# Optimization experiments

Measured on AMD Instinct MI355X. Metric: run time of the kernel, lower is better.

## Reference

```python
import jax, jax.numpy as jnp
import numpy as np

NUM_BITS = 1024
DIM = 128
SIGMA = 0.1
MU = 0.0


def setup_inputs() -> dict:
    key = jax.random.key(0)
    k1, k2, k3 = jax.random.split(key, 3)
    emb1 = jax.random.normal(k1, (4096, DIM), dtype=jnp.float32)
    emb2 = jax.random.normal(k2, (8192, DIM), dtype=jnp.float32)
    r = jax.random.normal(k3, (NUM_BITS, DIM), dtype=jnp.float32) * SIGMA + MU
    pi = jnp.array([np.pi], dtype=jnp.float32)
    return {"emb1": emb1, "emb2": emb2, "r": r, "pi": pi}


def reference(emb1, emb2, r, pi):
    d = r.shape[0]  # num_bits
    # LSH: random projection then binarize (sign bits as 0/1 floats)
    u = (emb1 @ r.T > 0).astype(jnp.float32)  # [N1, d]
    v = (emb2 @ r.T > 0).astype(jnp.float32)  # [N2, d]
    # cdist(p=0) on binary codes == Hamming distance.
    # For binary u,v: sum(u != v) = sum(u) + sum(v) - 2 * u @ v.T
    su = jnp.sum(u, axis=-1, keepdims=True)        # [N1, 1]
    sv = jnp.sum(v, axis=-1)                       # [N2]
    hamming = su + sv[None, :] - 2.0 * (u @ v.T)   # [N1, N2]
    return jnp.cos((pi[0] / d) * hamming)
```

## Files before the change

### kernel.cpp

```cpp
#include <hip/hip_runtime.h>
#include <hip/hip_bf16.h>
#include <stdint.h>


#define NBITS   1024
#define NROWS1  4096
#define NROWS2  8192

__global__ __launch_bounds__(256, 3) void lsh_project_pack(
    const float4* __restrict__ emb1,
    const float4* __restrict__ emb2,
    const float4* __restrict__ r4,
    unsigned long long* __restrict__ packed)
{
  __shared__ float4 e_lds[32 * 32];
  __shared__ float4 r_lds[256 * 8];

  const int t = threadIdx.x;
  const int w = t >> 6;
  const int l = t & 63;
  const int rowBlk  = blockIdx.x;
  const int bitTile = blockIdx.y;

  const int rowStart = rowBlk * 32;
  const bool side1   = rowStart < NROWS1;
  const float4* __restrict__ eb4 = side1 ? emb1 : emb2;
  const int rowOff = side1 ? rowStart : rowStart - NROWS1;

#pragma unroll
  for (int i = 0; i < 4; ++i) {
    const int idx = t + i * 256;
    e_lds[idx] = eb4[rowOff * 32 + idx];
  }

  float acc[8][4];
#pragma unroll
  for (int r = 0; r < 8; ++r)
#pragma unroll
    for (int p = 0; p < 4; ++p) acc[r][p] = 0.0f;

  const int key = l & 7;

  for (int ch = 0; ch < 4; ++ch) {
    __syncthreads();
#pragma unroll
    for (int i = 0; i < 8; ++i) {
      const int idx = t + i * 256;
      const int bit = idx >> 3;
      const int s   = idx & 7;
      r_lds[bit * 8 + (s ^ (bit & 7))] =
          r4[(size_t)(bitTile * 256 + bit) * 32 + ch * 8 + s];
    }
    __syncthreads();

#pragma unroll
    for (int ks = 0; ks < 8; ++ks) {
      float4 rv[4];
#pragma unroll
      for (int p = 0; p < 4; ++p)
        rv[p] = r_lds[(p * 64 + l) * 8 + (ks ^ key)];
      float4 ev[8];
#pragma unroll
      for (int r = 0; r < 8; ++r)
        ev[r] = e_lds[(w * 8 + r) * 32 + ch * 8 + ks];
#pragma unroll
      for (int r = 0; r < 8; ++r)
#pragma unroll
        for (int p = 0; p < 4; ++p) {
          acc[r][p] = fmaf(ev[r].x, rv[p].x, acc[r][p]);
          acc[r][p] = fmaf(ev[r].y, rv[p].y, acc[r][p]);
          acc[r][p] = fmaf(ev[r].z, rv[p].z, acc[r][p]);
          acc[r][p] = fmaf(ev[r].w, rv[p].w, acc[r][p]);
        }
    }
  }

  unsigned long long myword = 0;
#pragma unroll
  for (int r = 0; r < 8; ++r)
#pragma unroll
    for (int p = 0; p < 4; ++p) {
      const unsigned long long m = __ballot(acc[r][p] > 0.0f);
      if (l == r * 4 + p) myword = m;
    }
  if (l < 32) {
    const int row = rowStart + w * 8 + (l >> 2);
    packed[(size_t)row * 16 + bitTile * 4 + (l & 3)] = myword;
  }
}

__global__ __launch_bounds__(256, 3) void lsh_hamming_cos(
    const uint4* __restrict__ up,
    const uint4* __restrict__ vp,
    const float* __restrict__ pi_in,
    float* __restrict__ out)
{
  __shared__ uint4 u_lds[64 * 8];
  __shared__ uint4 v_lds[256 * 8];

  const int t  = threadIdx.x;
  const int w  = t >> 6;
  const int l  = t & 63;
  const int n0 = blockIdx.x * 256;
  const int m0 = blockIdx.y * 64;

#pragma unroll
  for (int i = 0; i < 2; ++i)
    u_lds[t + i * 256] = up[(size_t)m0 * 8 + t + i * 256];

#pragma unroll
  for (int i = 0; i < 8; ++i) {
    const int idx = t + i * 256;
    const int col = idx >> 3;
    const int w4  = idx & 7;
    v_lds[col * 8 + (w4 ^ ((col >> 2) & 7))] = vp[(size_t)n0 * 8 + idx];
  }
  __syncthreads();

  int h[8][8];
#pragma unroll
  for (int r = 0; r < 8; ++r)
#pragma unroll
    for (int j = 0; j < 8; ++j) h[r][j] = 0;

  const int key  = l & 7;
  const int row0 = w * 16 + (l >> 5) * 8;
  const int c0   = (l & 31) * 4;

#pragma unroll
  for (int kk = 0; kk < 8; ++kk) {
    uint4 U[8];
#pragma unroll
    for (int r = 0; r < 8; ++r)
      U[r] = u_lds[(row0 + r) * 8 + kk];
    const int slot = kk ^ key;
#pragma unroll
    for (int half = 0; half < 2; ++half) {
#pragma unroll
      for (int j = 0; j < 4; ++j) {
        const uint4 V = v_lds[(c0 + half * 128 + j) * 8 + slot];
#pragma unroll
        for (int r = 0; r < 8; ++r) {
          int s = h[r][half * 4 + j];
          s += __builtin_popcount(U[r].x ^ V.x);
          s += __builtin_popcount(U[r].y ^ V.y);
          s += __builtin_popcount(U[r].z ^ V.z);
          s += __builtin_popcount(U[r].w ^ V.w);
          h[r][half * 4 + j] = s;
        }
      }
    }
  }

  const float scale = pi_in[0] * (1.0f / (float)NBITS);

#pragma unroll
  for (int r = 0; r < 8; ++r) {
    const size_t row = (size_t)(m0 + row0 + r);
#pragma unroll
    for (int half = 0; half < 2; ++half) {
      float4 o;
      o.x = __cosf(scale * (float)h[r][half * 4 + 0]);
      o.y = __cosf(scale * (float)h[r][half * 4 + 1]);
      o.z = __cosf(scale * (float)h[r][half * 4 + 2]);
      o.w = __cosf(scale * (float)h[r][half * 4 + 3]);
      *(float4*)(out + row * NROWS2 + n0 + c0 + half * 128) = o;
    }
  }
}

extern "C" void kernel_launch(void* const* d_in, const int* in_sizes, int n_in,
                              void* d_out, int out_size, void* d_ws, size_t ws_size,
                              hipStream_t stream) {
  const float* emb1 = (const float*)d_in[0];
  const float* emb2 = (const float*)d_in[1];
  const float* r    = (const float*)d_in[2];
  const float* pi   = (const float*)d_in[3];

  unsigned long long* packed = (unsigned long long*)d_ws;

  dim3 g1(384, 4), b1(256);
  lsh_project_pack<<<g1, b1, 0, stream>>>(
      (const float4*)emb1, (const float4*)emb2, (const float4*)r, packed);

  dim3 g2(32, 64), b2(256);
  lsh_hamming_cos<<<g2, b2, 0, stream>>>(
      (const uint4*)packed,
      (const uint4*)(packed + (size_t)NROWS1 * 16),
      pi, (float*)d_out);
}
```

Measured before the change: 239.4 us.

## Restructure projection to per-thread rows with scalar r loads; fuse popcount-add

The projection kernel drops its LDS tiling. Each thread now owns one embedding row and accumulates 64 projection bits in registers. The r rows are wave-uniform, so they are read through readfirstlane scalar loads, and the sign bits are packed per thread instead of with ballots. This removes the LDS staging and barriers, but adds register pressure (64 accumulators plus staged operands) under a tighter launch bound, which risks spills. The Hamming kernel uses inline v_bcnt_u32_b32 asm so each popcount and accumulate is a single instruction.

```diff
diff --git a/kernel.cpp b/kernel.cpp
--- a/kernel.cpp
+++ b/kernel.cpp
@@ -7,86 +7,83 @@
 #define NROWS1  4096
 #define NROWS2  8192
 
-__global__ __launch_bounds__(256, 3) void lsh_project_pack(
+__global__ __launch_bounds__(256, 4) void lsh_project_pack(
     const float4* __restrict__ emb1,
     const float4* __restrict__ emb2,
     const float4* __restrict__ r4,
     unsigned long long* __restrict__ packed)
 {
-  __shared__ float4 e_lds[32 * 32];
-  __shared__ float4 r_lds[256 * 8];
+  const int t      = threadIdx.x;
+  const int rowBlk = blockIdx.x;
+  const int word   = blockIdx.y;
 
-  const int t = threadIdx.x;
-  const int w = t >> 6;
-  const int l = t & 63;
-  const int rowBlk  = blockIdx.x;
-  const int bitTile = blockIdx.y;
-
-  const int rowStart = rowBlk * 32;
+  const int rowStart = rowBlk * 256;
   const bool side1   = rowStart < NROWS1;
   const float4* __restrict__ eb4 = side1 ? emb1 : emb2;
-  const int rowOff = side1 ? rowStart : rowStart - NROWS1;
+  const int rowLoc = (side1 ? rowStart : rowStart - NROWS1) + t;
+  const int bit0   = word * 64;
+
+  float acc[64];
+#pragma unroll
+  for (int b = 0; b < 64; ++b) acc[b] = 0.0f;
+
+  for (int ch = 0; ch < 4; ++ch) {
+    float4 E[8];
+#pragma unroll
+    for (int c = 0; c < 8; ++c)
+      E[c] = eb4[(size_t)rowLoc * 32 + ch * 8 + c];
+
+    float4 ra[8], rb[8];
+    {
+      const int s0 = __builtin_amdgcn_readfirstlane(bit0 * 32 + ch * 8);
+#pragma unroll
+      for (int c = 0; c < 8; ++c) ra[c] = r4[s0 + c];
+    }
 
 #pragma unroll
-  for (int i = 0; i < 4; ++i) {
-    const int idx = t + i * 256;
-    e_lds[idx] = eb4[rowOff * 32 + idx];
-  }
-
-  float acc[8][4];
+    for (int b = 0; b < 64; b += 2) {
+      {
+        const int s1 =
+            __builtin_amdgcn_readfirstlane((bit0 + b + 1) * 32 + ch * 8);
 #pragma unroll
-  for (int r = 0; r < 8; ++r)
+        for (int c = 0; c < 8; ++c) rb[c] = r4[s1 + c];
+      }
 #pragma unroll
-    for (int p = 0; p < 4; ++p) acc[r][p] = 0.0f;
-
-  const int key = l & 7;
-
-  for (int ch = 0; ch < 4; ++ch) {
-    __syncthreads();
+      for (int c = 0; c < 8; ++c) {
+        acc[b] = fmaf(E[c].x, ra[c].x, acc[b]);
+        acc[b] = fmaf(E[c].y, ra[c].y, acc[b]);
+        acc[b] = fmaf(E[c].z, ra[c].z, acc[b]);
+        acc[b] = fmaf(E[c].w, ra[c].w, acc[b]);
+      }
+      if (b + 2 < 64) {
+        const int s2 =
+            __builtin_amdgcn_readfirstlane((bit0 + b + 2) * 32 + ch * 8);
 #pragma unroll
-    for (int i = 0; i < 8; ++i) {
-      const int idx = t + i * 256;
-      const int bit = idx >> 3;
-      const int s   = idx & 7;
-      r_lds[bit * 8 + (s ^ (bit & 7))] =
-          r4[(size_t)(bitTile * 256 + bit) * 32 + ch * 8 + s];
-    }
-    __syncthreads();
-
+        for (int c = 0; c < 8; ++c) ra[c] = r4[s2 + c];
+      }
 #pragma unroll
-    for (int ks = 0; ks < 8; ++ks) {
-      float4 rv[4];
-#pragma unroll
-      for (int p = 0; p < 4; ++p)
-        rv[p] = r_lds[(p * 64 + l) * 8 + (ks ^ key)];
-      float4 ev[8];
-#pragma unroll
-      for (int r = 0; r < 8; ++r)
-        ev[r] = e_lds[(w * 8 + r) * 32 + ch * 8 + ks];
-#pragma unroll
-      for (int r = 0; r < 8; ++r)
-#pragma unroll
-        for (int p = 0; p < 4; ++p) {
-          acc[r][p] = fmaf(ev[r].x, rv[p].x, acc[r][p]);
-          acc[r][p] = fmaf(ev[r].y, rv[p].y, acc[r][p]);
-          acc[r][p] = fmaf(ev[r].z, rv[p].z, acc[r][p]);
-          acc[r][p] = fmaf(ev[r].w, rv[p].w, acc[r][p]);
-        }
+      for (int c = 0; c < 8; ++c) {
+        acc[b + 1] = fmaf(E[c].x, rb[c].x, acc[b + 1]);
+        acc[b + 1] = fmaf(E[c].y, rb[c].y, acc[b + 1]);
+        acc[b + 1] = fmaf(E[c].z, rb[c].z, acc[b + 1]);
+        acc[b + 1] = fmaf(E[c].w, rb[c].w, acc[b + 1]);
+      }
     }
   }
 
-  unsigned long long myword = 0;
+  unsigned int w0 = 0, w1 = 0;
 #pragma unroll
-  for (int r = 0; r < 8; ++r)
+  for (int b = 0; b < 32; ++b) w0 |= (acc[b] > 0.0f) ? (1u << b) : 0u;
 #pragma unroll
-    for (int p = 0; p < 4; ++p) {
-      const unsigned long long m = __ballot(acc[r][p] > 0.0f);
-      if (l == r * 4 + p) myword = m;
-    }
-  if (l < 32) {
-    const int row = rowStart + w * 8 + (l >> 2);
-    packed[(size_t)row * 16 + bitTile * 4 + (l & 3)] = myword;
-  }
+  for (int b = 0; b < 32; ++b) w1 |= (acc[32 + b] > 0.0f) ? (1u << b) : 0u;
+
+  const int grow = rowStart + t;
+  uint2 wv; wv.x = w0; wv.y = w1;
+  *(uint2*)&packed[(size_t)grow * 16 + word] = wv;
+}
+
+__device__ __forceinline__ void bcnt_acc(unsigned int& h, unsigned int x) {
+  asm("v_bcnt_u32_b32 %0, %1, %0" : "+v"(h) : "v"(x));
 }
 
 __global__ __launch_bounds__(256, 3) void lsh_hamming_cos(
@@ -117,11 +114,11 @@
   }
   __syncthreads();
 
-  int h[8][8];
+  unsigned int h[8][8];
 #pragma unroll
   for (int r = 0; r < 8; ++r)
 #pragma unroll
-    for (int j = 0; j < 8; ++j) h[r][j] = 0;
+    for (int j = 0; j < 8; ++j) h[r][j] = 0u;
 
   const int key  = l & 7;
   const int row0 = w * 16 + (l >> 5) * 8;
@@ -141,12 +138,11 @@
         const uint4 V = v_lds[(c0 + half * 128 + j) * 8 + slot];
 #pragma unroll
         for (int r = 0; r < 8; ++r) {
-          int s = h[r][half * 4 + j];
-          s += __builtin_popcount(U[r].x ^ V.x);
-          s += __builtin_popcount(U[r].y ^ V.y);
-          s += __builtin_popcount(U[r].z ^ V.z);
-          s += __builtin_popcount(U[r].w ^ V.w);
-          h[r][half * 4 + j] = s;
+          unsigned int& s = h[r][half * 4 + j];
+          bcnt_acc(s, U[r].x ^ V.x);
+          bcnt_acc(s, U[r].y ^ V.y);
+          bcnt_acc(s, U[r].z ^ V.z);
+          bcnt_acc(s, U[r].w ^ V.w);
         }
       }
     }
@@ -179,7 +175,7 @@
 
   unsigned long long* packed = (unsigned long long*)d_ws;
 
-  dim3 g1(384, 4), b1(256);
+  dim3 g1(48, 16), b1(256);
   lsh_project_pack<<<g1, b1, 0, stream>>>(
       (const float4*)emb1, (const float4*)emb2, (const float4*)r, packed);
 
```

After: 353.5 us. 1.48x slower.

## Restructure projection kernel to hold r rows in registers with scalar embedding loads

Applied to the files above, without the earlier changes.

The projection/pack kernel now keeps each lane's full 128-float row of r in registers and streams embedding rows through wave-uniform (readfirstlane) scalar loads, dropping all LDS staging and barriers. Each wave processes 64 rows serially, ballots the sign bits per row, and each lane stores one packed 64-bit word. This removes the shared-memory traffic and syncs, but holds 128 VGPRs per lane for r, relies on the scalar cache to serve the embedding reads, and makes each wave's 64-row loop strictly sequential.

```diff
diff --git a/kernel.cpp b/kernel.cpp
--- a/kernel.cpp
+++ b/kernel.cpp
@@ -8,85 +8,51 @@
 #define NROWS2  8192
 
 __global__ __launch_bounds__(256, 3) void lsh_project_pack(
-    const float4* __restrict__ emb1,
-    const float4* __restrict__ emb2,
+    const float* __restrict__ emb1,
+    const float* __restrict__ emb2,
     const float4* __restrict__ r4,
     unsigned long long* __restrict__ packed)
 {
-  __shared__ float4 e_lds[32 * 32];
-  __shared__ float4 r_lds[256 * 8];
-
   const int t = threadIdx.x;
   const int w = t >> 6;
   const int l = t & 63;
-  const int rowBlk  = blockIdx.x;
-  const int bitTile = blockIdx.y;
+  const int word = blockIdx.y;
 
-  const int rowStart = rowBlk * 32;
-  const bool side1   = rowStart < NROWS1;
-  const float4* __restrict__ eb4 = side1 ? emb1 : emb2;
-  const int rowOff = side1 ? rowStart : rowStart - NROWS1;
+  const int blockRow0 = blockIdx.x * 256;
+  const bool side1    = blockRow0 < NROWS1;
+  const float* __restrict__ ebase = side1 ? emb1 : emb2;
+  const int localRow0 = (side1 ? blockRow0 : blockRow0 - NROWS1) + w * 64;
 
+  float4 R[32];
+  {
+    const float4* __restrict__ rrow = r4 + (size_t)(word * 64 + l) * 32;
 #pragma unroll
-  for (int i = 0; i < 4; ++i) {
-    const int idx = t + i * 256;
-    e_lds[idx] = eb4[rowOff * 32 + idx];
+    for (int c = 0; c < 32; ++c) R[c] = rrow[c];
   }
 
-  float acc[8][4];
+  unsigned long long keep = 0ull;
+
+  for (int i = 0; i < 64; ++i) {
+    const int rowU = __builtin_amdgcn_readfirstlane(localRow0 + i);
+    const float* __restrict__ p = ebase + (size_t)rowU * 128;
+
+    float s0 = 0.0f, s1 = 0.0f, s2 = 0.0f, s3 = 0.0f;
 #pragma unroll
-  for (int r = 0; r < 8; ++r)
-#pragma unroll
-    for (int p = 0; p < 4; ++p) acc[r][p] = 0.0f;
+    for (int c = 0; c < 32; ++c) {
+      const float4 rv = R[c];
+      s0 = fmaf(p[c * 4 + 0], rv.x, s0);
+      s1 = fmaf(p[c * 4 + 1], rv.y, s1);
+      s2 = fmaf(p[c * 4 + 2], rv.z, s2);
+      s3 = fmaf(p[c * 4 + 3], rv.w, s3);
+    }
+    const float sum = (s0 + s1) + (s2 + s3);
 
-  const int key = l & 7;
-
-  for (int ch = 0; ch < 4; ++ch) {
-    __syncthreads();
-#pragma unroll
-    for (int i = 0; i < 8; ++i) {
-      const int idx = t + i * 256;
-      const int bit = idx >> 3;
-      const int s   = idx & 7;
-      r_lds[bit * 8 + (s ^ (bit & 7))] =
-          r4[(size_t)(bitTile * 256 + bit) * 32 + ch * 8 + s];
-    }
-    __syncthreads();
-
-#pragma unroll
-    for (int ks = 0; ks < 8; ++ks) {
-      float4 rv[4];
-#pragma unroll
-      for (int p = 0; p < 4; ++p)
-        rv[p] = r_lds[(p * 64 + l) * 8 + (ks ^ key)];
-      float4 ev[8];
-#pragma unroll
-      for (int r = 0; r < 8; ++r)
-        ev[r] = e_lds[(w * 8 + r) * 32 + ch * 8 + ks];
-#pragma unroll
-      for (int r = 0; r < 8; ++r)
-#pragma unroll
-        for (int p = 0; p < 4; ++p) {
-          acc[r][p] = fmaf(ev[r].x, rv[p].x, acc[r][p]);
-          acc[r][p] = fmaf(ev[r].y, rv[p].y, acc[r][p]);
-          acc[r][p] = fmaf(ev[r].z, rv[p].z, acc[r][p]);
-          acc[r][p] = fmaf(ev[r].w, rv[p].w, acc[r][p]);
-        }
-    }
+    const unsigned long long m = __ballot(sum > 0.0f);
+    keep = (i == l) ? m : keep;
   }
 
-  unsigned long long myword = 0;
-#pragma unroll
-  for (int r = 0; r < 8; ++r)
-#pragma unroll
-    for (int p = 0; p < 4; ++p) {
-      const unsigned long long m = __ballot(acc[r][p] > 0.0f);
-      if (l == r * 4 + p) myword = m;
-    }
-  if (l < 32) {
-    const int row = rowStart + w * 8 + (l >> 2);
-    packed[(size_t)row * 16 + bitTile * 4 + (l & 3)] = myword;
-  }
+  const int growRow = blockRow0 + w * 64 + l;
+  packed[(size_t)growRow * 16 + word] = keep;
 }
 
 __global__ __launch_bounds__(256, 3) void lsh_hamming_cos(
@@ -179,9 +145,9 @@
 
   unsigned long long* packed = (unsigned long long*)d_ws;
 
-  dim3 g1(384, 4), b1(256);
+  dim3 g1(48, 16), b1(256);
   lsh_project_pack<<<g1, b1, 0, stream>>>(
-      (const float4*)emb1, (const float4*)emb2, (const float4*)r, packed);
+      emb1, emb2, (const float4*)r, packed);
 
   dim3 g2(32, 64), b2(256);
   lsh_hamming_cos<<<g2, b2, 0, stream>>>(
```

Measured after the change: 321.5 us. 34.3% more time.

## Enlarge projection kernel register tile to 16 rows by 8 bit-groups

Applied to the files above, without the earlier changes.

The projection/pack kernel now computes a 64-row by 512-bit tile per block instead of 32 by 256, with each thread holding a 16x8 accumulator grid. Embedding rows are staged per k-chunk rather than all at once. The grid shrinks to 192x2 blocks and launch bounds drop to 2 blocks per CU. The goal is higher FMA-to-LDS-load ratio and less redundant global traffic, at the cost of more registers, lower occupancy, and fewer blocks to fill the GPU.

```diff
diff --git a/kernel.cpp b/kernel.cpp
--- a/kernel.cpp
+++ b/kernel.cpp
@@ -7,14 +7,14 @@
 #define NROWS1  4096
 #define NROWS2  8192
 
-__global__ __launch_bounds__(256, 3) void lsh_project_pack(
+__global__ __launch_bounds__(256, 2) void lsh_project_pack(
     const float4* __restrict__ emb1,
     const float4* __restrict__ emb2,
     const float4* __restrict__ r4,
     unsigned long long* __restrict__ packed)
 {
-  __shared__ float4 e_lds[32 * 32];
-  __shared__ float4 r_lds[256 * 8];
+  __shared__ float4 e_lds[64 * 8];
+  __shared__ float4 r_lds[512 * 8];
 
   const int t = threadIdx.x;
   const int w = t >> 6;
@@ -22,71 +22,73 @@
   const int rowBlk  = blockIdx.x;
   const int bitTile = blockIdx.y;
 
-  const int rowStart = rowBlk * 32;
-  const bool side1   = rowStart < NROWS1;
+  const int blockRow0 = rowBlk * 64;
+  const bool side1    = blockRow0 < NROWS1;
   const float4* __restrict__ eb4 = side1 ? emb1 : emb2;
-  const int rowOff = side1 ? rowStart : rowStart - NROWS1;
+  const int rowOff = side1 ? blockRow0 : blockRow0 - NROWS1;
 
+  float acc[16][8];
 #pragma unroll
-  for (int i = 0; i < 4; ++i) {
-    const int idx = t + i * 256;
-    e_lds[idx] = eb4[rowOff * 32 + idx];
-  }
-
-  float acc[8][4];
+  for (int rr = 0; rr < 16; ++rr)
 #pragma unroll
-  for (int r = 0; r < 8; ++r)
-#pragma unroll
-    for (int p = 0; p < 4; ++p) acc[r][p] = 0.0f;
+    for (int p = 0; p < 8; ++p) acc[rr][p] = 0.0f;
 
   const int key = l & 7;
 
   for (int ch = 0; ch < 4; ++ch) {
     __syncthreads();
 #pragma unroll
-    for (int i = 0; i < 8; ++i) {
+    for (int i = 0; i < 2; ++i) {
+      const int idx = t + i * 256;
+      const int row = idx >> 3;
+      const int ks  = idx & 7;
+      e_lds[idx] = eb4[(size_t)(rowOff + row) * 32 + ch * 8 + ks];
+    }
+#pragma unroll
+    for (int i = 0; i < 16; ++i) {
       const int idx = t + i * 256;
       const int bit = idx >> 3;
       const int s   = idx & 7;
       r_lds[bit * 8 + (s ^ (bit & 7))] =
-          r4[(size_t)(bitTile * 256 + bit) * 32 + ch * 8 + s];
+          r4[(size_t)(bitTile * 512 + bit) * 32 + ch * 8 + s];
     }
     __syncthreads();
 
 #pragma unroll
     for (int ks = 0; ks < 8; ++ks) {
-      float4 rv[4];
+      float4 rv[8];
 #pragma unroll
-      for (int p = 0; p < 4; ++p)
+      for (int p = 0; p < 8; ++p)
         rv[p] = r_lds[(p * 64 + l) * 8 + (ks ^ key)];
-      float4 ev[8];
 #pragma unroll
-      for (int r = 0; r < 8; ++r)
-        ev[r] = e_lds[(w * 8 + r) * 32 + ch * 8 + ks];
+      for (int rr = 0; rr < 16; ++rr) {
+        const float4 ev = e_lds[(w * 16 + rr) * 8 + ks];
 #pragma unroll
-      for (int r = 0; r < 8; ++r)
-#pragma unroll
-        for (int p = 0; p < 4; ++p) {
-          acc[r][p] = fmaf(ev[r].x, rv[p].x, acc[r][p]);
-          acc[r][p] = fmaf(ev[r].y, rv[p].y, acc[r][p]);
-          acc[r][p] = fmaf(ev[r].z, rv[p].z, acc[r][p]);
-          acc[r][p] = fmaf(ev[r].w, rv[p].w, acc[r][p]);
+        for (int p = 0; p < 8; ++p) {
+          acc[rr][p] = fmaf(ev.x, rv[p].x, acc[rr][p]);
+          acc[rr][p] = fmaf(ev.y, rv[p].y, acc[rr][p]);
+          acc[rr][p] = fmaf(ev.z, rv[p].z, acc[rr][p]);
+          acc[rr][p] = fmaf(ev.w, rv[p].w, acc[rr][p]);
         }
+      }
     }
   }
 
-  unsigned long long myword = 0;
+  unsigned long long keepA = 0ull, keepB = 0ull;
 #pragma unroll
-  for (int r = 0; r < 8; ++r)
+  for (int rr = 0; rr < 16; ++rr)
 #pragma unroll
-    for (int p = 0; p < 4; ++p) {
-      const unsigned long long m = __ballot(acc[r][p] > 0.0f);
-      if (l == r * 4 + p) myword = m;
+    for (int p = 0; p < 8; ++p) {
+      const unsigned long long m = __ballot(acc[rr][p] > 0.0f);
+      const int id = rr * 8 + p;
+      if (id < 64) { if (l == id)      keepA = m; }
+      else         { if (l == id - 64) keepB = m; }
     }
-  if (l < 32) {
-    const int row = rowStart + w * 8 + (l >> 2);
-    packed[(size_t)row * 16 + bitTile * 4 + (l & 3)] = myword;
-  }
+
+  const int rowA = blockRow0 + w * 16 + (l >> 3);
+  const int word = bitTile * 8 + (l & 7);
+  packed[(size_t)rowA * 16 + word]       = keepA;
+  packed[(size_t)(rowA + 8) * 16 + word] = keepB;
 }
 
 __global__ __launch_bounds__(256, 3) void lsh_hamming_cos(
@@ -179,7 +181,7 @@
 
   unsigned long long* packed = (unsigned long long*)d_ws;
 
-  dim3 g1(384, 4), b1(256);
+  dim3 g1(192, 2), b1(256);
   lsh_project_pack<<<g1, b1, 0, stream>>>(
       (const float4*)emb1, (const float4*)emb2, (const float4*)r, packed);
 
```

After: 298.6 us. 24.7% more time.
